# Kernel tuning notes

Hardware: AMD Instinct MI355X
Metric: run time of the kernel (lower is better)

Reference implementation:

```python
import jax, jax.numpy as jnp
import numpy as np

N = 50000          # number of graph nodes
R = 4              # number of relation types (rt_num)
E = 800000         # edges per relation (avg degree 16)
D_IN = 128
D_OUT = 64
EPS = 1e-12        # torch F.normalize eps


def setup_inputs() -> dict:
    key = jax.random.key(0)
    k1, k2, k3, k4, k5 = jax.random.split(key, 5)
    x = jax.random.normal(k1, (N, D_IN), dtype=jnp.float32)
    W = jax.random.normal(k2, (R, D_IN, D_OUT), dtype=jnp.float32)
    b = jnp.zeros((R, D_OUT), dtype=jnp.float32)
    adj_vals = jax.random.uniform(k3, (R, E), dtype=jnp.float32)
    adj_rows = jax.random.randint(k4, (R, E), 0, N, dtype=jnp.int32)
    adj_cols = jax.random.randint(k5, (R, E), 0, N, dtype=jnp.int32)
    return {"x": x, "W": W, "b": b, "adj_vals": adj_vals,
            "adj_rows": adj_rows, "adj_cols": adj_cols, "dropout": 0}


def reference(x, W, b, adj_vals, adj_rows, adj_cols, dropout):
    # dropout == 0 -> F.dropout is the identity; reference is deterministic.
    # Per-relation dense projection: xw[r] = x @ W[r]   -> [R, N, D_OUT]
    xw = jnp.einsum('nd,rdo->rno', x, W)

    def per_relation(xw_r, rows_r, cols_r, vals_r, b_r):
        # sparse adjacency SpMM: out[i] = sum_e vals[e] * xw[cols[e]] for rows[e]==i
        msg = xw_r[cols_r] * vals_r[:, None]                  # [E, D_OUT] gather
        agg = jax.ops.segment_sum(msg, rows_r, num_segments=N)  # [N, D_OUT] scatter-add
        return jax.nn.relu(agg + b_r)                          # bias + act

    outs = jax.vmap(per_relation)(xw, adj_rows, adj_cols, adj_vals, b)  # [R, N, D_OUT]
    total = jnp.sum(outs, axis=0)                               # cross-relation sum
    # L2 normalize over feature dim (torch F.normalize, dim=1)
    norm = jnp.maximum(jnp.linalg.norm(total, axis=1, keepdims=True), EPS)
    return total / norm
```

## Files before the change

### kernel.cpp

```cpp
#include <hip/hip_runtime.h>
#include <hip/hip_bf16.h>
#include <stdint.h>

#define NN 50000
#define DI 128
#define DO 64
#define NE 800000
#define NR 4
#define NB 782
#define NBUCK (NR*NB)
#define PCHUNK 7168
#define PWG ((NE + PCHUNK - 1) / PCHUNK)
#define RSCAP 4096
#define GEMMB ((NN + 127) / 128)

typedef short short8 __attribute__((ext_vector_type(8)));
typedef float f32x4  __attribute__((ext_vector_type(4)));
union FragU { uint4 u; short8 s; };

__device__ __forceinline__ uint32_t bfb(float f)
{
    __hip_bfloat16 h = __float2bfloat16(f);
    return (uint32_t)*reinterpret_cast<unsigned short*>(&h);
}

template<int N, int PER, int BLK>
__device__ inline void block_exscan(int* a)
{
    __shared__ int wsum[BLK / 64];
    int tid = threadIdx.x;
    int base = tid * PER;
    int v[PER]; int s = 0;
    #pragma unroll
    for (int j = 0; j < PER; ++j) {
        int idx = base + j;
        int x = (idx < N) ? a[idx] : 0;
        v[j] = s; s += x;
    }
    int lane = tid & 63, wv = tid >> 6;
    int inc = s;
    #pragma unroll
    for (int off = 1; off < 64; off <<= 1) {
        int u = __shfl_up(inc, off);
        if (lane >= off) inc += u;
    }
    if (lane == 63) wsum[wv] = inc;
    __syncthreads();
    int woff = 0;
    for (int w = 0; w < wv; ++w) woff += wsum[w];
    int tb = woff + inc - s;
    #pragma unroll
    for (int j = 0; j < PER; ++j) {
        int idx = base + j;
        if (idx < N) a[idx] = tb + v[j];
    }
}

__global__ __launch_bounds__(256) void prep_kernel(
    const float* __restrict__ W, const int* __restrict__ rows,
    uint16_t* __restrict__ wt, int* __restrict__ gtot)
{
    __shared__ int h[NB];
    int bid = blockIdx.x, tid = threadIdx.x;

    if (bid < 128) {
        int i = bid * 256 + tid;
        int r = i >> 13;
        int k = (i >> 6) & 127;
        int n = i & 63;
        wt[((size_t)(r * DO + n) << 7) + k] = (uint16_t)bfb(W[i]);
    } else {
        int bb = bid - 128;
        int r = bb >> 5, sub = bb & 31;
        for (int i = tid; i < NB; i += 256) h[i] = 0;
        __syncthreads();
        const int4* rr4 = (const int4*)(rows + (size_t)r * NE);
        for (int k = sub * 256 + tid; k < NE / 4; k += 32 * 256) {
            int4 v = rr4[k];
            atomicAdd(&h[v.x >> 6], 1);
            atomicAdd(&h[v.y >> 6], 1);
            atomicAdd(&h[v.z >> 6], 1);
            atomicAdd(&h[v.w >> 6], 1);
        }
        __syncthreads();
        int* gt = gtot + r * NB;
        for (int i = tid; i < NB; i += 256)
            if (h[i]) atomicAdd(&gt[i], h[i]);
    }
}

__global__ __launch_bounds__(512) void bases_kernel(
    const int* __restrict__ gtot, int* __restrict__ gstart,
    int* __restrict__ gcur)
{
    __shared__ int a[NBUCK + 1];
    int tid = threadIdx.x;
    for (int i = tid; i < NBUCK + 1; i += 512) a[i] = (i < NBUCK) ? gtot[i] : 0;
    __syncthreads();
    block_exscan<NBUCK + 1, 7, 512>(a);
    __syncthreads();
    for (int i = tid; i < NBUCK + 1; i += 512) {
        gstart[i] = a[i];
        if (i < NBUCK) gcur[i] = a[i];
    }
}

__global__ __launch_bounds__(512) void gemm_place_kernel(
    const float* __restrict__ x, const uint4* __restrict__ wt4,
    uint16_t* __restrict__ xwb,
    const int* __restrict__ rows, const int* __restrict__ cols,
    const float* __restrict__ vals, int* __restrict__ gcur,
    int2* __restrict__ csr)
{
    __shared__ __align__(16) char smem[63616];
    int tid = threadIdx.x;

    if (blockIdx.x < GEMMB) {
        uint16_t* tile = (uint16_t*)smem;
        int wv = __builtin_amdgcn_readfirstlane(tid >> 6);
        int lane = tid & 63;
        int n0 = blockIdx.x * 128 + wv * 16;
        int m16 = lane & 15, g = lane >> 4;
        bool act = (n0 < NN);

        FragU af[4];
        if (act) {
            const float4* x4 = (const float4*)x;
            size_t rb = ((size_t)(n0 + m16) * DI) >> 2;
            #pragma unroll
            for (int ks = 0; ks < 4; ++ks) {
                float4 f0 = x4[rb + ks * 8 + g * 2];
                float4 f1 = x4[rb + ks * 8 + g * 2 + 1];
                af[ks].u.x = bfb(f0.x) | (bfb(f0.y) << 16);
                af[ks].u.y = bfb(f0.z) | (bfb(f0.w) << 16);
                af[ks].u.z = bfb(f1.x) | (bfb(f1.y) << 16);
                af[ks].u.w = bfb(f1.z) | (bfb(f1.w) << 16);
            }
        }

        int nrows = NN - blockIdx.x * 128; if (nrows > 128) nrows = 128;

        for (int r = 0; r < NR; ++r) {
            if (act) {
                #pragma unroll
                for (int ct = 0; ct < 4; ++ct) {
                    f32x4 acc = {0.f, 0.f, 0.f, 0.f};
                    #pragma unroll
                    for (int ks = 0; ks < 4; ++ks) {
                        FragU b;
                        b.u = wt4[(size_t)((r * DO + ct * 16 + m16) * 16) + ks * 4 + g];
                        acc = __builtin_amdgcn_mfma_f32_16x16x32_bf16(
                            af[ks].s, b.s, acc, 0, 0, 0);
                    }
                    #pragma unroll
                    for (int j = 0; j < 4; ++j)
                        tile[(wv * 16 + g * 4 + j) * 64 + ct * 16 + m16] =
                            (uint16_t)bfb(acc[j]);
                }
            }
            __syncthreads();
            uint4* dst = (uint4*)(xwb + ((size_t)r * NN + blockIdx.x * 128) * 64);
            int tot = nrows * 8;
            for (int i = tid; i < tot; i += 512)
                dst[i] = ((const uint4*)tile)[i];
            __syncthreads();
        }
        return;
    }

    int* lofs  = (int*)smem;
    int* gbase = (int*)(smem + 3136);
    int2* stag = (int2*)(smem + 6272);
    int pb = blockIdx.x - GEMMB;
    int r = pb / PWG;
    int chunk = pb - r * PWG;
    int e0 = chunk * PCHUNK;
    int cnt = NE - e0; if (cnt > PCHUNK) cnt = PCHUNK;
    const int*   rr = rows + (size_t)r * NE + e0;
    const int*   cc = cols + (size_t)r * NE + e0;
    const float* vv = vals + (size_t)r * NE + e0;

    for (int i = tid; i <= NB; i += 512) lofs[i] = 0;
    __syncthreads();
    for (int k = tid; k < cnt; k += 512) atomicAdd(&lofs[rr[k] >> 6], 1);
    __syncthreads();
    block_exscan<NB + 1, 2, 512>(lofs);
    __syncthreads();
    for (int b = tid; b < NB; b += 512) {
        int c = lofs[b + 1] - lofs[b];
        if (c > 0) gbase[b] = atomicAdd(&gcur[r * NB + b], c);
    }
    __syncthreads();
    for (int k = tid; k < cnt; k += 512) {
        int row = rr[k];
        int b = row >> 6;
        int slot = atomicAdd(&lofs[b], 1);
        stag[slot] = make_int2((cc[k] & 0xFFFF) | ((row & 63) << 16) | (b << 22),
                               __float_as_int(vv[k]));
    }
    __syncthreads();
    for (int i = tid; i < cnt; i += 512) {
        int2 t = stag[i];
        unsigned b2 = ((unsigned)t.x) >> 22;
        int start = b2 ? lofs[b2 - 1] : 0;
        csr[gbase[b2] + (i - start)] = t;
    }
}

__global__ __launch_bounds__(256) void rowsort_kernel(
    int2* __restrict__ csr, const int* __restrict__ gstart,
    int* __restrict__ rowptr)
{
    __shared__ int2 stag[RSCAP];
    __shared__ int cnt[64];
    __shared__ int ofs[64];
    int blk = blockIdx.x;
    int r   = blockIdx.y;
    int b   = r * NB + blk;
    int s = gstart[b], e = gstart[b + 1];
    int cntE = e - s; if (cntE > RSCAP) cntE = RSCAP;
    int tid = threadIdx.x;
    if (tid < 64) cnt[tid] = 0;
    __syncthreads();

    int2 ed[RSCAP / 256];
    #pragma unroll
    for (int j = 0; j < RSCAP / 256; ++j) {
        int i = tid + j * 256;
        if (i < cntE) {
            ed[j] = csr[s + i];
            atomicAdd(&cnt[(ed[j].x >> 16) & 63], 1);
        }
    }
    __syncthreads();
    if (tid < 64) {
        int c = cnt[tid];
        int inc = c;
        #pragma unroll
        for (int off = 1; off < 64; off <<= 1) {
            int u = __shfl_up(inc, off);
            if (tid >= off) inc += u;
        }
        ofs[tid] = inc - c;
        int n = blk * 64 + tid;
        if (n < NN) rowptr[(size_t)r * NN + n] = s + inc - c;
        if (b == NBUCK - 1 && tid == 0)
            rowptr[(size_t)NR * NN] = gstart[NBUCK];
    }
    __syncthreads();
    #pragma unroll
    for (int j = 0; j < RSCAP / 256; ++j) {
        int i = tid + j * 256;
        if (i < cntE) {
            int rl = (ed[j].x >> 16) & 63;
            int slot = atomicAdd(&ofs[rl], 1);
            stag[slot] = ed[j];
        }
    }
    __syncthreads();
    for (int i = tid; i < cntE; i += 256) {
        int2 t = stag[i];
        t.x = (r * NN + (t.x & 0xFFFF)) << 4;
        csr[s + i] = t;
    }
}

struct Stage {
    float v[NR];
    uint2 u[NR];
};

__device__ __forceinline__ void stage_issue(
    int k, const int* dege, const int* ofsv, const float* valv,
    const uint2* __restrict__ xw2, int e4, int fq, Stage& st)
{
    #pragma unroll
    for (int r = 0; r < NR; ++r) {
        if (k < dege[r]) {
            int ec = k + e4;
            int ofs  = __shfl(ofsv[r], ec);
            float vv = __shfl(valv[r], ec);
            st.v[r] = vv;
            st.u[r] = xw2[ofs + fq];
        } else {
            st.v[r] = 0.f;
            st.u[r] = make_uint2(0u, 0u);
        }
    }
}

__device__ __forceinline__ void stage_consume(const Stage& st, float a[NR][4])
{
    #pragma unroll
    for (int r = 0; r < NR; ++r) {
        float v = st.v[r];
        a[r][0] = fmaf(v, __uint_as_float(st.u[r].x << 16),          a[r][0]);
        a[r][1] = fmaf(v, __uint_as_float(st.u[r].x & 0xFFFF0000u),  a[r][1]);
        a[r][2] = fmaf(v, __uint_as_float(st.u[r].y << 16),          a[r][2]);
        a[r][3] = fmaf(v, __uint_as_float(st.u[r].y & 0xFFFF0000u),  a[r][3]);
    }
}

__global__ __launch_bounds__(256) void spmm_fused_kernel(
    const uint2* __restrict__ xw2, const int2* __restrict__ csr,
    const int* __restrict__ rowptr, const float* __restrict__ bias,
    float* __restrict__ out)
{
    int n = __builtin_amdgcn_readfirstlane(
        (int)((blockIdx.x * 256 + threadIdx.x) >> 6));
    int lane = threadIdx.x & 63;
    int e4 = lane >> 4, fq = lane & 15;
    if (n >= NN) return;

    int dege[NR]; int ofsv[NR]; float valv[NR];
    int sbeg[NR], send[NR];
    int maxdeg = 0;
    #pragma unroll
    for (int r = 0; r < NR; ++r) {
        sbeg[r] = rowptr[(size_t)r * NN + n];
        send[r] = rowptr[(size_t)r * NN + n + 1];
        int d = send[r] - sbeg[r];
        if (d > 64) d = 64;
        int2 cv = (lane < d) ? csr[sbeg[r] + lane] : make_int2(0, 0);
        ofsv[r] = cv.x;
        valv[r] = __int_as_float(cv.y);
        dege[r] = (d + 3) & ~3;
        maxdeg = max(maxdeg, dege[r]);
    }

    float a[NR][4];
    #pragma unroll
    for (int r = 0; r < NR; ++r)
        #pragma unroll
        for (int j = 0; j < 4; ++j) a[r][j] = 0.f;

    Stage A, B;
    stage_issue(0, dege, ofsv, valv, xw2, e4, fq, A);
    for (int k = 0; k < maxdeg; k += 8) {
        stage_issue(k + 4, dege, ofsv, valv, xw2, e4, fq, B);
        stage_consume(A, a);
        stage_issue(k + 8, dege, ofsv, valv, xw2, e4, fq, A);
        stage_consume(B, a);
    }

    #pragma unroll
    for (int r = 0; r < NR; ++r) {
        for (int i = sbeg[r] + 64; i < send[r]; ++i) {
            int2 cv = csr[i];
            float v = (lane < 16) ? __int_as_float(cv.y) : 0.f;
            uint2 u = xw2[cv.x + fq];
            a[r][0] = fmaf(v, __uint_as_float(u.x << 16),         a[r][0]);
            a[r][1] = fmaf(v, __uint_as_float(u.x & 0xFFFF0000u), a[r][1]);
            a[r][2] = fmaf(v, __uint_as_float(u.y << 16),         a[r][2]);
            a[r][3] = fmaf(v, __uint_as_float(u.y & 0xFFFF0000u), a[r][3]);
        }
    }

    float t[4] = {0.f, 0.f, 0.f, 0.f};
    #pragma unroll
    for (int r = 0; r < NR; ++r) {
        #pragma unroll
        for (int j = 0; j < 4; ++j) {
            a[r][j] += __shfl_xor(a[r][j], 16);
            a[r][j] += __shfl_xor(a[r][j], 32);
        }
        float4 br = *(const float4*)&bias[r * DO + 4 * fq];
        t[0] += fmaxf(a[r][0] + br.x, 0.f);
        t[1] += fmaxf(a[r][1] + br.y, 0.f);
        t[2] += fmaxf(a[r][2] + br.z, 0.f);
        t[3] += fmaxf(a[r][3] + br.w, 0.f);
    }
    float s2 = t[0]*t[0] + t[1]*t[1] + t[2]*t[2] + t[3]*t[3];
    #pragma unroll
    for (int off = 8; off >= 1; off >>= 1) s2 += __shfl_xor(s2, off);
    float inv = 1.0f / fmaxf(sqrtf(s2), 1e-12f);
    if (lane < 16) {
        float4 o = make_float4(t[0]*inv, t[1]*inv, t[2]*inv, t[3]*inv);
        *(float4*)&out[(size_t)n * DO + 4 * fq] = o;
    }
}

__global__ __launch_bounds__(256) void gemm_kernel(
    const float* __restrict__ x, const float* __restrict__ W,
    __hip_bfloat16* __restrict__ xwb)
{
    __shared__ float Wl[DI * DO];
    for (int i = threadIdx.x; i < DI * DO; i += 256) Wl[i] = W[i];
    __syncthreads();

    int wv   = __builtin_amdgcn_readfirstlane((int)(threadIdx.x >> 6));
    int lane = threadIdx.x & 63;
    int n0   = blockIdx.x * 32 + wv * 8;
    if (n0 >= NN) return;
    int nrows = NN - n0; if (nrows > 8) nrows = 8;

    if (nrows == 8) {
        const float* xr = x + (size_t)n0 * DI;
        float acc[8] = {0.f,0.f,0.f,0.f,0.f,0.f,0.f,0.f};
        #pragma unroll 8
        for (int k = 0; k < DI; ++k) {
            float w = Wl[k * DO + lane];
            #pragma unroll
            for (int rr = 0; rr < 8; ++rr)
                acc[rr] = fmaf(xr[(size_t)rr * DI + k], w, acc[rr]);
        }
        #pragma unroll
        for (int rr = 0; rr < 8; ++rr)
            xwb[(size_t)(n0 + rr) * DO + lane] = __float2bfloat16(acc[rr]);
    } else {
        for (int rr = 0; rr < nrows; ++rr) {
            const float* xr = x + (size_t)(n0 + rr) * DI;
            float acc = 0.f;
            for (int k = 0; k < DI; ++k)
                acc = fmaf(xr[k], Wl[k * DO + lane], acc);
            xwb[(size_t)(n0 + rr) * DO + lane] = __float2bfloat16(acc);
        }
    }
}

__global__ __launch_bounds__(256) void scatter_kernel(
    const __hip_bfloat16* __restrict__ xwb, const float* __restrict__ vals,
    const int* __restrict__ rows, const int* __restrict__ cols,
    float* __restrict__ agg)
{
    const int nPairs = NE / 2;
    int gwave  = (blockIdx.x * 256 + threadIdx.x) >> 6;
    int half   = (threadIdx.x >> 5) & 1;
    int l32    = threadIdx.x & 31;
    int stride = gridDim.x * 4;
    const uint16_t* xw16 = reinterpret_cast<const uint16_t*>(xwb);
    for (int p = gwave; p < nPairs; p += stride) {
        int e = 2 * p + half;
        int row = rows[e]; int col = cols[e]; float v = vals[e];
        uint32_t packed = *reinterpret_cast<const uint32_t*>(
            xw16 + ((size_t)col << 6) + 2 * l32);
        float f0 = __uint_as_float(packed << 16);
        float f1 = __uint_as_float(packed & 0xFFFF0000u);
        float* dst = agg + ((size_t)row << 6) + 2 * l32;
        atomicAdd(dst,     v * f0);
        atomicAdd(dst + 1, v * f1);
    }
}

__global__ __launch_bounds__(256) void accum_kernel(
    float* __restrict__ agg, const float* __restrict__ b,
    float* __restrict__ out, int first)
{
    int i = blockIdx.x * 256 + threadIdx.x;
    if (i >= NN * DO) return;
    float v = agg[i] + b[i & (DO - 1)];
    agg[i] = 0.f;
    v = fmaxf(v, 0.f);
    out[i] = first ? v : (out[i] + v);
}

__global__ __launch_bounds__(256) void norm_kernel(float* __restrict__ out)
{
    int n = (blockIdx.x * 256 + threadIdx.x) >> 6;
    int lane = threadIdx.x & 63;
    if (n >= NN) return;
    size_t idx = (size_t)n * DO + lane;
    float t = out[idx];
    float s = t * t;
    #pragma unroll
    for (int off = 32; off >= 1; off >>= 1) s += __shfl_xor(s, off);
    out[idx] = t / fmaxf(sqrtf(s), 1e-12f);
}

extern "C" void kernel_launch(void* const* d_in, const int* in_sizes, int n_in,
                              void* d_out, int out_size, void* d_ws, size_t ws_size,
                              hipStream_t stream)
{
    const float* x    = (const float*)d_in[0];
    const float* W    = (const float*)d_in[1];
    const float* b    = (const float*)d_in[2];
    const float* vals = (const float*)d_in[3];
    const int*   rows = (const int*)d_in[4];
    const int*   cols = (const int*)d_in[5];
    float* out = (float*)d_out;
    char* ws = (char*)d_ws;

    const size_t O_XW = 0;
    const size_t O_CS = O_XW + (size_t)NR * NN * DO * 2;
    const size_t O_RP = O_CS + (size_t)NR * NE * 8;
    const size_t O_GT = O_RP + ((size_t)NR * NN + 4) * 4;
    const size_t O_GS = O_GT + (size_t)NBUCK * 4;
    const size_t O_GC = O_GS + (size_t)(NBUCK + 1) * 4;
    const size_t O_WT = O_GC + (size_t)NBUCK * 4;
    const size_t NEED = O_WT + 65536;

    if (ws_size >= NEED) {
        __hip_bfloat16* xwb = (__hip_bfloat16*)(ws + O_XW);
        int2* csr   = (int2*)(ws + O_CS);
        int* rowptr = (int*)(ws + O_RP);
        int* gtot   = (int*)(ws + O_GT);
        int* gstart = (int*)(ws + O_GS);
        int* gcur   = (int*)(ws + O_GC);
        uint16_t* wt = (uint16_t*)(ws + O_WT);

        hipMemsetAsync(gtot, 0, (size_t)NBUCK * 4, stream);
        prep_kernel<<<dim3(256), dim3(256), 0, stream>>>(W, rows, wt, gtot);
        bases_kernel<<<dim3(1), dim3(512), 0, stream>>>(gtot, gstart, gcur);
        gemm_place_kernel<<<dim3(GEMMB + PWG * NR), dim3(512), 0, stream>>>(
            x, (const uint4*)wt, (uint16_t*)xwb,
            rows, cols, vals, gcur, csr);
        rowsort_kernel<<<dim3(NB, NR), dim3(256), 0, stream>>>(csr, gstart, rowptr);
        spmm_fused_kernel<<<dim3((NN * 64 + 255) / 256), dim3(256), 0, stream>>>(
            (const uint2*)xwb, csr, rowptr, b, out);
    } else {
        __hip_bfloat16* xwb = (__hip_bfloat16*)ws;
        float* agg = (float*)(ws + (size_t)NN * DO * 2);
        hipMemsetAsync(agg, 0, (size_t)NN * DO * 4, stream);
        for (int r = 0; r < NR; ++r) {
            gemm_kernel<<<dim3((NN + 31) / 32), dim3(256), 0, stream>>>(
                x, W + (size_t)r * DI * DO, xwb);
            scatter_kernel<<<dim3(2048), dim3(256), 0, stream>>>(
                xwb, vals + (size_t)r * NE, rows + (size_t)r * NE,
                cols + (size_t)r * NE, agg);
            accum_kernel<<<dim3((NN * DO + 255) / 256), dim3(256), 0, stream>>>(
                agg, b + (size_t)r * DO, out, r == 0);
        }
        norm_kernel<<<dim3((NN * DO + 255) / 256), dim3(256), 0, stream>>>(out);
    }
}
```

Baseline: 171.9 us.

## Fuse per-bucket row sort into SpMM kernel using shared-memory edge buffers

Removes the separate rowsort kernel and the global rowptr array. Each 512-thread block now loads the bucketed edges for its 64 rows across all four relations into LDS, counting-sorts them by local row there, and then runs the gathered SpMM, bias, ReLU and normalize for 8 rows per wave. This drops one launch and the global write/read of the sorted CSR and rowptr. In exchange LDS use per block is large, which limits occupancy. Only 782 blocks are launched, and an overflow path rescans the global bucket per row when a bucket exceeds ECAP.

```diff
diff --git a/kernel.cpp b/kernel.cpp
--- a/kernel.cpp
+++ b/kernel.cpp
@@ -11,8 +11,8 @@
 #define NBUCK (NR*NB)
 #define PCHUNK 7168
 #define PWG ((NE + PCHUNK - 1) / PCHUNK)
-#define RSCAP 4096
 #define GEMMB ((NN + 127) / 128)
+#define ECAP 1408
 
 typedef short short8 __attribute__((ext_vector_type(8)));
 typedef float f32x4  __attribute__((ext_vector_type(4)));
@@ -207,176 +207,184 @@
     }
 }
 
-__global__ __launch_bounds__(256) void rowsort_kernel(
-    int2* __restrict__ csr, const int* __restrict__ gstart,
-    int* __restrict__ rowptr)
-{
-    __shared__ int2 stag[RSCAP];
-    __shared__ int cnt[64];
-    __shared__ int ofs[64];
-    int blk = blockIdx.x;
-    int r   = blockIdx.y;
-    int b   = r * NB + blk;
-    int s = gstart[b], e = gstart[b + 1];
-    int cntE = e - s; if (cntE > RSCAP) cntE = RSCAP;
-    int tid = threadIdx.x;
-    if (tid < 64) cnt[tid] = 0;
-    __syncthreads();
-
-    int2 ed[RSCAP / 256];
-    #pragma unroll
-    for (int j = 0; j < RSCAP / 256; ++j) {
-        int i = tid + j * 256;
-        if (i < cntE) {
-            ed[j] = csr[s + i];
-            atomicAdd(&cnt[(ed[j].x >> 16) & 63], 1);
-        }
-    }
-    __syncthreads();
-    if (tid < 64) {
-        int c = cnt[tid];
+__global__ __launch_bounds__(512) void spmm2_kernel(
+    const uint2* __restrict__ xw2, const int2* __restrict__ csr,
+    const int* __restrict__ gstart, const float* __restrict__ bias,
+    float* __restrict__ out)
+{
+    __shared__ int2 ebuf[NR][ECAP];
+    __shared__ int rcnt[NR][64];
+    __shared__ int rofs[NR][64];
+    __shared__ int rcur[NR][64];
+    int tid = threadIdx.x, blk = blockIdx.x;
+    int wv = __builtin_amdgcn_readfirstlane(tid >> 6);
+    int lane = tid & 63;
+
+    if (tid < 256) rcnt[tid >> 6][tid & 63] = 0;
+    __syncthreads();
+
+    int sbeg[NR], cnt[NR], scnt[NR];
+    int2 ed[NR][3];
+    #pragma unroll
+    for (int r = 0; r < NR; ++r) {
+        int b = r * NB + blk;
+        sbeg[r] = gstart[b];
+        cnt[r]  = gstart[b + 1] - sbeg[r];
+        scnt[r] = cnt[r] > ECAP ? ECAP : cnt[r];
+        #pragma unroll
+        for (int j = 0; j < 3; ++j) {
+            int i = tid + j * 512;
+            if (i < scnt[r]) {
+                ed[r][j] = csr[sbeg[r] + i];
+                atomicAdd(&rcnt[r][(ed[r][j].x >> 16) & 63], 1);
+            }
+        }
+    }
+    __syncthreads();
+
+    if (wv < NR) {
+        int c = rcnt[wv][lane];
         int inc = c;
         #pragma unroll
         for (int off = 1; off < 64; off <<= 1) {
             int u = __shfl_up(inc, off);
-            if (tid >= off) inc += u;
-        }
-        ofs[tid] = inc - c;
-        int n = blk * 64 + tid;
-        if (n < NN) rowptr[(size_t)r * NN + n] = s + inc - c;
-        if (b == NBUCK - 1 && tid == 0)
-            rowptr[(size_t)NR * NN] = gstart[NBUCK];
-    }
-    __syncthreads();
-    #pragma unroll
-    for (int j = 0; j < RSCAP / 256; ++j) {
-        int i = tid + j * 256;
-        if (i < cntE) {
-            int rl = (ed[j].x >> 16) & 63;
-            int slot = atomicAdd(&ofs[rl], 1);
-            stag[slot] = ed[j];
-        }
-    }
-    __syncthreads();
-    for (int i = tid; i < cntE; i += 256) {
-        int2 t = stag[i];
-        t.x = (r * NN + (t.x & 0xFFFF)) << 4;
-        csr[s + i] = t;
-    }
-}
-
-struct Stage {
-    float v[NR];
-    uint2 u[NR];
-};
-
-__device__ __forceinline__ void stage_issue(
-    int k, const int* dege, const int* ofsv, const float* valv,
-    const uint2* __restrict__ xw2, int e4, int fq, Stage& st)
-{
+            if (lane >= off) inc += u;
+        }
+        rofs[wv][lane] = inc - c;
+        rcur[wv][lane] = inc - c;
+    }
+    __syncthreads();
+
     #pragma unroll
     for (int r = 0; r < NR; ++r) {
-        if (k < dege[r]) {
-            int ec = k + e4;
-            int ofs  = __shfl(ofsv[r], ec);
-            float vv = __shfl(valv[r], ec);
-            st.v[r] = vv;
-            st.u[r] = xw2[ofs + fq];
-        } else {
-            st.v[r] = 0.f;
-            st.u[r] = make_uint2(0u, 0u);
-        }
-    }
-}
-
-__device__ __forceinline__ void stage_consume(const Stage& st, float a[NR][4])
-{
-    #pragma unroll
-    for (int r = 0; r < NR; ++r) {
-        float v = st.v[r];
-        a[r][0] = fmaf(v, __uint_as_float(st.u[r].x << 16),          a[r][0]);
-        a[r][1] = fmaf(v, __uint_as_float(st.u[r].x & 0xFFFF0000u),  a[r][1]);
-        a[r][2] = fmaf(v, __uint_as_float(st.u[r].y << 16),          a[r][2]);
-        a[r][3] = fmaf(v, __uint_as_float(st.u[r].y & 0xFFFF0000u),  a[r][3]);
-    }
-}
-
-__global__ __launch_bounds__(256) void spmm_fused_kernel(
-    const uint2* __restrict__ xw2, const int2* __restrict__ csr,
-    const int* __restrict__ rowptr, const float* __restrict__ bias,
-    float* __restrict__ out)
-{
-    int n = __builtin_amdgcn_readfirstlane(
-        (int)((blockIdx.x * 256 + threadIdx.x) >> 6));
-    int lane = threadIdx.x & 63;
+        #pragma unroll
+        for (int j = 0; j < 3; ++j) {
+            int i = tid + j * 512;
+            if (i < scnt[r]) {
+                int rl = (ed[r][j].x >> 16) & 63;
+                int slot = atomicAdd(&rcur[r][rl], 1);
+                ebuf[r][slot] = make_int2((r * NN + (ed[r][j].x & 0xFFFF)) << 4,
+                                          ed[r][j].y);
+            }
+        }
+    }
+    __syncthreads();
+
     int e4 = lane >> 4, fq = lane & 15;
-    if (n >= NN) return;
-
-    int dege[NR]; int ofsv[NR]; float valv[NR];
-    int sbeg[NR], send[NR];
-    int maxdeg = 0;
-    #pragma unroll
-    for (int r = 0; r < NR; ++r) {
-        sbeg[r] = rowptr[(size_t)r * NN + n];
-        send[r] = rowptr[(size_t)r * NN + n + 1];
-        int d = send[r] - sbeg[r];
-        if (d > 64) d = 64;
-        int2 cv = (lane < d) ? csr[sbeg[r] + lane] : make_int2(0, 0);
-        ofsv[r] = cv.x;
-        valv[r] = __int_as_float(cv.y);
-        dege[r] = (d + 3) & ~3;
-        maxdeg = max(maxdeg, dege[r]);
-    }
-
-    float a[NR][4];
+    float4 br[NR];
     #pragma unroll
     for (int r = 0; r < NR; ++r)
-        #pragma unroll
-        for (int j = 0; j < 4; ++j) a[r][j] = 0.f;
-
-    Stage A, B;
-    stage_issue(0, dege, ofsv, valv, xw2, e4, fq, A);
-    for (int k = 0; k < maxdeg; k += 8) {
-        stage_issue(k + 4, dege, ofsv, valv, xw2, e4, fq, B);
-        stage_consume(A, a);
-        stage_issue(k + 8, dege, ofsv, valv, xw2, e4, fq, A);
-        stage_consume(B, a);
-    }
-
-    #pragma unroll
-    for (int r = 0; r < NR; ++r) {
-        for (int i = sbeg[r] + 64; i < send[r]; ++i) {
-            int2 cv = csr[i];
-            float v = (lane < 16) ? __int_as_float(cv.y) : 0.f;
-            uint2 u = xw2[cv.x + fq];
-            a[r][0] = fmaf(v, __uint_as_float(u.x << 16),         a[r][0]);
-            a[r][1] = fmaf(v, __uint_as_float(u.x & 0xFFFF0000u), a[r][1]);
-            a[r][2] = fmaf(v, __uint_as_float(u.y << 16),         a[r][2]);
-            a[r][3] = fmaf(v, __uint_as_float(u.y & 0xFFFF0000u), a[r][3]);
-        }
-    }
-
-    float t[4] = {0.f, 0.f, 0.f, 0.f};
-    #pragma unroll
-    for (int r = 0; r < NR; ++r) {
-        #pragma unroll
-        for (int j = 0; j < 4; ++j) {
-            a[r][j] += __shfl_xor(a[r][j], 16);
-            a[r][j] += __shfl_xor(a[r][j], 32);
-        }
-        float4 br = *(const float4*)&bias[r * DO + 4 * fq];
-        t[0] += fmaxf(a[r][0] + br.x, 0.f);
-        t[1] += fmaxf(a[r][1] + br.y, 0.f);
-        t[2] += fmaxf(a[r][2] + br.z, 0.f);
-        t[3] += fmaxf(a[r][3] + br.w, 0.f);
-    }
-    float s2 = t[0]*t[0] + t[1]*t[1] + t[2]*t[2] + t[3]*t[3];
-    #pragma unroll
-    for (int off = 8; off >= 1; off >>= 1) s2 += __shfl_xor(s2, off);
-    float inv = 1.0f / fmaxf(sqrtf(s2), 1e-12f);
-    if (lane < 16) {
-        float4 o = make_float4(t[0]*inv, t[1]*inv, t[2]*inv, t[3]*inv);
-        *(float4*)&out[(size_t)n * DO + 4 * fq] = o;
+        br[r] = *(const float4*)&bias[r * DO + 4 * fq];
+
+    for (int mi = 0; mi < 8; ++mi) {
+        int m = wv * 8 + mi;
+        int n = blk * 64 + m;
+        if (n >= NN) break;
+
+        int st[NR], dc[NR], dege[NR];
+        int maxdeg = 0;
+        #pragma unroll
+        for (int r = 0; r < NR; ++r) {
+            st[r] = rofs[r][m];
+            dc[r] = rcnt[r][m];
+            dege[r] = (dc[r] + 3) & ~3;
+            maxdeg = max(maxdeg, dege[r]);
+        }
+
+        float a[NR][4];
+        #pragma unroll
+        for (int r = 0; r < NR; ++r)
+            #pragma unroll
+            for (int j = 0; j < 4; ++j) a[r][j] = 0.f;
+
+        float vA[NR]; uint2 uA[NR];
+        float vB[NR]; uint2 uB[NR];
+
+        #pragma unroll
+        for (int r = 0; r < NR; ++r) {
+            if (0 < dege[r]) {
+                int e = e4; int ec = e < dc[r] ? e : dc[r] - 1;
+                int2 cv = ebuf[r][st[r] + ec];
+                vA[r] = (e < dc[r]) ? __int_as_float(cv.y) : 0.f;
+                uA[r] = xw2[cv.x + fq];
+            } else { vA[r] = 0.f; uA[r] = make_uint2(0u, 0u); }
+        }
+        for (int k = 0; k < maxdeg; k += 8) {
+            #pragma unroll
+            for (int r = 0; r < NR; ++r) {
+                int kk = k + 4;
+                if (kk < dege[r]) {
+                    int e = kk + e4; int ec = e < dc[r] ? e : dc[r] - 1;
+                    int2 cv = ebuf[r][st[r] + ec];
+                    vB[r] = (e < dc[r]) ? __int_as_float(cv.y) : 0.f;
+                    uB[r] = xw2[cv.x + fq];
+                } else { vB[r] = 0.f; uB[r] = make_uint2(0u, 0u); }
+            }
+            #pragma unroll
+            for (int r = 0; r < NR; ++r) {
+                float v = vA[r];
+                a[r][0] = fmaf(v, __uint_as_float(uA[r].x << 16),         a[r][0]);
+                a[r][1] = fmaf(v, __uint_as_float(uA[r].x & 0xFFFF0000u), a[r][1]);
+                a[r][2] = fmaf(v, __uint_as_float(uA[r].y << 16),         a[r][2]);
+                a[r][3] = fmaf(v, __uint_as_float(uA[r].y & 0xFFFF0000u), a[r][3]);
+            }
+            #pragma unroll
+            for (int r = 0; r < NR; ++r) {
+                int kk = k + 8;
+                if (kk < dege[r]) {
+                    int e = kk + e4; int ec = e < dc[r] ? e : dc[r] - 1;
+                    int2 cv = ebuf[r][st[r] + ec];
+                    vA[r] = (e < dc[r]) ? __int_as_float(cv.y) : 0.f;
+                    uA[r] = xw2[cv.x + fq];
+                } else { vA[r] = 0.f; uA[r] = make_uint2(0u, 0u); }
+            }
+            #pragma unroll
+            for (int r = 0; r < NR; ++r) {
+                float v = vB[r];
+                a[r][0] = fmaf(v, __uint_as_float(uB[r].x << 16),         a[r][0]);
+                a[r][1] = fmaf(v, __uint_as_float(uB[r].x & 0xFFFF0000u), a[r][1]);
+                a[r][2] = fmaf(v, __uint_as_float(uB[r].y << 16),         a[r][2]);
+                a[r][3] = fmaf(v, __uint_as_float(uB[r].y & 0xFFFF0000u), a[r][3]);
+            }
+        }
+
+        #pragma unroll
+        for (int r = 0; r < NR; ++r) {
+            if (cnt[r] > ECAP) {
+                for (int i = sbeg[r] + ECAP; i < sbeg[r] + cnt[r]; ++i) {
+                    int2 cv = csr[i];
+                    int rl = (cv.x >> 16) & 63;
+                    float v = (rl == m && lane < 16) ? __int_as_float(cv.y) : 0.f;
+                    uint2 u = xw2[(((size_t)r * NN + (cv.x & 0xFFFF)) << 4) + fq];
+                    a[r][0] = fmaf(v, __uint_as_float(u.x << 16),         a[r][0]);
+                    a[r][1] = fmaf(v, __uint_as_float(u.x & 0xFFFF0000u), a[r][1]);
+                    a[r][2] = fmaf(v, __uint_as_float(u.y << 16),         a[r][2]);
+                    a[r][3] = fmaf(v, __uint_as_float(u.y & 0xFFFF0000u), a[r][3]);
+                }
+            }
+        }
+
+        float t[4] = {0.f, 0.f, 0.f, 0.f};
+        #pragma unroll
+        for (int r = 0; r < NR; ++r) {
+            #pragma unroll
+            for (int j = 0; j < 4; ++j) {
+                a[r][j] += __shfl_xor(a[r][j], 16);
+                a[r][j] += __shfl_xor(a[r][j], 32);
+            }
+            t[0] += fmaxf(a[r][0] + br[r].x, 0.f);
+            t[1] += fmaxf(a[r][1] + br[r].y, 0.f);
+            t[2] += fmaxf(a[r][2] + br[r].z, 0.f);
+            t[3] += fmaxf(a[r][3] + br[r].w, 0.f);
+        }
+        float s2 = t[0]*t[0] + t[1]*t[1] + t[2]*t[2] + t[3]*t[3];
+        #pragma unroll
+        for (int off = 8; off >= 1; off >>= 1) s2 += __shfl_xor(s2, off);
+        float inv = 1.0f / fmaxf(sqrtf(s2), 1e-12f);
+        if (lane < 16) {
+            float4 o = make_float4(t[0]*inv, t[1]*inv, t[2]*inv, t[3]*inv);
+            *(float4*)&out[(size_t)n * DO + 4 * fq] = o;
+        }
     }
 }
 
@@ -482,8 +490,7 @@
 
     const size_t O_XW = 0;
     const size_t O_CS = O_XW + (size_t)NR * NN * DO * 2;
-    const size_t O_RP = O_CS + (size_t)NR * NE * 8;
-    const size_t O_GT = O_RP + ((size_t)NR * NN + 4) * 4;
+    const size_t O_GT = O_CS + (size_t)NR * NE * 8;
     const size_t O_GS = O_GT + (size_t)NBUCK * 4;
     const size_t O_GC = O_GS + (size_t)(NBUCK + 1) * 4;
     const size_t O_WT = O_GC + (size_t)NBUCK * 4;
@@ -492,7 +499,6 @@
     if (ws_size >= NEED) {
         __hip_bfloat16* xwb = (__hip_bfloat16*)(ws + O_XW);
         int2* csr   = (int2*)(ws + O_CS);
-        int* rowptr = (int*)(ws + O_RP);
         int* gtot   = (int*)(ws + O_GT);
         int* gstart = (int*)(ws + O_GS);
         int* gcur   = (int*)(ws + O_GC);
@@ -504,9 +510,8 @@
         gemm_place_kernel<<<dim3(GEMMB + PWG * NR), dim3(512), 0, stream>>>(
             x, (const uint4*)wt, (uint16_t*)xwb,
             rows, cols, vals, gcur, csr);
-        rowsort_kernel<<<dim3(NB, NR), dim3(256), 0, stream>>>(csr, gstart, rowptr);
-        spmm_fused_kernel<<<dim3((NN * 64 + 255) / 256), dim3(256), 0, stream>>>(
-            (const uint2*)xwb, csr, rowptr, b, out);
+        spmm2_kernel<<<dim3(NB), dim3(512), 0, stream>>>(
+            (const uint2*)xwb, csr, gstart, b, out);
     } else {
         __hip_bfloat16* xwb = (__hip_bfloat16*)ws;
         float* agg = (float*)(ws + (size_t)NN * DO * 2);
```

New measurement: 162.7 us, median of 2. -5.4%, faster.
